# Performance work log

Hardware: AMD Instinct MI355X
Metric: run time of the kernel (lower is better)

## Reference

```python
import jax, jax.numpy as jnp
import numpy as np
from jax import lax

N = 1024          # proposals per image
C = 81            # classes incl. background
F = 1024          # feature dim
K = 100           # detections_per_img
IMG_W, IMG_H = 1216.0, 800.0
SCORE_THRESH = 0.05
NMS_THRESH = 0.5
BBOX_CLIP = float(np.log(1000.0 / 16.0))
WX, WY, WW, WH = 10.0, 10.0, 5.0, 5.0     # BoxCoder default weights


def setup_inputs() -> dict:
    key = jax.random.key(0)
    k1, k2, k3, k4, k5 = jax.random.split(key, 5)
    class_logits = jax.random.normal(k1, (N, C), jnp.float32) * 2.0
    box_regression = jax.random.normal(k2, (N, C * 4), jnp.float32) * 0.2
    xy = jax.random.uniform(k3, (N, 2), jnp.float32) * jnp.array([IMG_W * 0.7, IMG_H * 0.7], jnp.float32)
    wh = 16.0 + jax.random.uniform(k4, (N, 2), jnp.float32) * jnp.array([IMG_W * 0.3, IMG_H * 0.3], jnp.float32)
    proposal_boxes = jnp.concatenate([xy, xy + wh], axis=1)  # valid xyxy
    features = jax.random.normal(k5, (N, F), jnp.float32)
    return {"class_logits": class_logits, "box_regression": box_regression,
            "proposal_boxes": proposal_boxes, "features": features}


def _decode(rel, boxes):
    # BoxCoder.decode with weights (10,10,5,5), TO_REMOVE=1. rel:[N,C*4] boxes:[N,4] -> [N,C,4]
    rel = rel.reshape(N, C, 4)
    widths = boxes[:, 2] - boxes[:, 0] + 1.0
    heights = boxes[:, 3] - boxes[:, 1] + 1.0
    ctr_x = boxes[:, 0] + 0.5 * widths
    ctr_y = boxes[:, 1] + 0.5 * heights
    dx = rel[..., 0] / WX
    dy = rel[..., 1] / WY
    dw = jnp.minimum(rel[..., 2] / WW, BBOX_CLIP)
    dh = jnp.minimum(rel[..., 3] / WH, BBOX_CLIP)
    pcx = dx * widths[:, None] + ctr_x[:, None]
    pcy = dy * heights[:, None] + ctr_y[:, None]
    pw = jnp.exp(dw) * widths[:, None]
    ph = jnp.exp(dh) * heights[:, None]
    return jnp.stack([pcx - 0.5 * pw, pcy - 0.5 * ph,
                      pcx + 0.5 * pw - 1.0, pcy + 0.5 * ph - 1.0], axis=-1)


def _clip(b):
    # clip_to_image with TO_REMOVE=1
    x1 = jnp.clip(b[..., 0], 0.0, IMG_W - 1.0)
    y1 = jnp.clip(b[..., 1], 0.0, IMG_H - 1.0)
    x2 = jnp.clip(b[..., 2], 0.0, IMG_W - 1.0)
    y2 = jnp.clip(b[..., 3], 0.0, IMG_H - 1.0)
    return jnp.stack([x1, y1, x2, y2], axis=-1)


def _nms_class(boxes_c, scores_c, valid_c):
    # Sequential hard NMS for one class with fixed shapes. Invalid (below score
    # thresh) boxes can neither be kept nor suppress others.
    s_sort = jnp.where(valid_c, scores_c, -jnp.inf)
    order = jnp.argsort(-s_sort)              # descending score
    b = boxes_c[order]
    v = valid_c[order]
    s = scores_c[order]
    area = (b[:, 2] - b[:, 0] + 1.0) * (b[:, 3] - b[:, 1] + 1.0)
    lt = jnp.maximum(b[:, None, :2], b[None, :, :2])
    rb = jnp.minimum(b[:, None, 2:], b[None, :, 2:])
    whd = jnp.clip(rb - lt + 1.0, 0.0)
    inter = whd[..., 0] * whd[..., 1]
    iou = inter / (area[:, None] + area[None, :] - inter)  # [N,N]
    idx = jnp.arange(N)
    def body(i, keep):
        sup = (iou[i] > NMS_THRESH) & keep[i] & (idx > i)
        return keep & ~sup
    keep = lax.fori_loop(0, N, body, v)
    return b, order, jnp.where(keep, s, -1.0)


def reference(class_logits, box_regression, proposal_boxes, features):
    probs = jax.nn.softmax(class_logits, axis=-1)          # [N,C]
    dec = _clip(_decode(box_regression, proposal_boxes))    # [N,C,4]
    boxes_cls = jnp.transpose(dec[:, 1:, :], (1, 0, 2))     # [C-1,N,4] (skip background)
    scores_cls = probs[:, 1:].T                             # [C-1,N]
    valid = scores_cls > SCORE_THRESH
    b_s, order, s_kept = jax.vmap(_nms_class)(boxes_cls, scores_cls, valid)
    flat_s = s_kept.reshape(-1)                             # [(C-1)*N]
    top_s, top_i = lax.top_k(flat_s, K)
    cls_i = top_i // N
    pos_i = top_i % N
    boxes_out = b_s[cls_i, pos_i]                           # [K,4]
    orig = order[cls_i, pos_i]                              # original proposal idx
    feat_out = features[orig]                               # [K,F]
    labels = cls_i + 1
    ok = top_s > 0.0
    scores_out = jnp.where(ok, top_s, 0.0)
    boxes_out = jnp.where(ok[:, None], boxes_out, 0.0)
    feat_out = jnp.where(ok[:, None], feat_out, 0.0)
    labels = jnp.where(ok, labels, 0)
    return boxes_out, scores_out, feat_out, labels
```

## Files before the change

kernel.cpp:

```cpp
#include <hip/hip_runtime.h>
#include <math.h>

#define N 1024
#define C 81
#define F 1024
#define K 100
#define NC1 80
#define MAXC (NC1 * N)
#define HBASE 0x3D00
#define HSIZE 1024
#define SELCAP 2048

#define SCORE_THRESH 0.05f
#define NMS_THRESH   0.5f
#define BBOX_CLIP    4.135166556742356f
#define IMG_W1       1215.0f
#define IMG_H1       799.0f

typedef unsigned long long u64;
typedef unsigned int u32;

__device__ float4 decode_box(const float* __restrict__ pboxes,
                             const float* __restrict__ boxreg, int idx, int cl)
{
    float4 pb = ((const float4*)pboxes)[idx];
    float4 r  = *(const float4*)(boxreg + (size_t)idx * (C * 4) + cl * 4);
    float w  = pb.z - pb.x + 1.0f, h = pb.w - pb.y + 1.0f;
    float cx = pb.x + 0.5f * w,  cy = pb.y + 0.5f * h;
    float dx = r.x / 10.0f, dy = r.y / 10.0f;
    float dw = fminf(r.z / 5.0f, BBOX_CLIP);
    float dh = fminf(r.w / 5.0f, BBOX_CLIP);
    float pcx = dx * w + cx, pcy = dy * h + cy;
    float pw = expf(dw) * w, ph = expf(dh) * h;
    float x1 = pcx - 0.5f * pw,        y1 = pcy - 0.5f * ph;
    float x2 = pcx + 0.5f * pw - 1.0f, y2 = pcy + 0.5f * ph - 1.0f;
    x1 = fminf(fmaxf(x1, 0.0f), IMG_W1);
    y1 = fminf(fmaxf(y1, 0.0f), IMG_H1);
    x2 = fminf(fmaxf(x2, 0.0f), IMG_W1);
    y2 = fminf(fmaxf(y2, 0.0f), IMG_H1);
    return make_float4(x1, y1, x2, y2);
}

__global__ __launch_bounds__(256) void k_softmax(
    const float* __restrict__ logits, float2* __restrict__ ms,
    int* __restrict__ hist, int* __restrict__ counter)
{
    int gid = blockIdx.x * 256 + threadIdx.x;
    if (gid < HSIZE) hist[gid] = 0;
    if (gid == 0) *counter = 0;

    int n = blockIdx.x * 4 + (threadIdx.x >> 6);
    int t = threadIdx.x & 63;

    float v1 = logits[n * C + t];
    float v2 = (t < C - 64) ? logits[n * C + 64 + t] : -INFINITY;
    float m = fmaxf(v1, v2);
    for (int off = 32; off; off >>= 1) m = fmaxf(m, __shfl_xor(m, off));
    float e1 = expf(v1 - m);
    float e2 = (t < C - 64) ? expf(v2 - m) : 0.0f;
    float s = e1 + e2;
    for (int off = 32; off; off >>= 1) s += __shfl_xor(s, off);

    if (t == 0) ms[n] = make_float2(m, s);
}

__global__ __launch_bounds__(256) void k_class(
    const float* __restrict__ logits, const float* __restrict__ boxreg,
    const float* __restrict__ pboxes, const float2* __restrict__ ms,
    u64* __restrict__ ckey, float4* __restrict__ cbox, int* __restrict__ corig,
    int* __restrict__ hist, int* __restrict__ counter)
{
    int c = blockIdx.x;
    int cl = c + 1;
    int t = threadIdx.x;
    __shared__ u64    skey64[N];
    __shared__ int    scnt[256];
    __shared__ float4 sbox[N];
    __shared__ float  sarea[N];
    __shared__ int    skeep[N];

    float2 p0 = ms[t],       p1 = ms[t + 256];
    float2 p2 = ms[t + 512], p3 = ms[t + 768];
    float s0 = expf(logits[(t      ) * C + cl] - p0.x) / p0.y;
    float s1 = expf(logits[(t + 256) * C + cl] - p1.x) / p1.y;
    float s2 = expf(logits[(t + 512) * C + cl] - p2.x) / p2.y;
    float s3 = expf(logits[(t + 768) * C + cl] - p3.x) / p3.y;
    int f0 = s0 > SCORE_THRESH, f1 = s1 > SCORE_THRESH;
    int f2 = s2 > SCORE_THRESH, f3 = s3 > SCORE_THRESH;
    int mycount = f0 + f1 + f2 + f3;
    scnt[t] = mycount;
    __syncthreads();
    for (int off = 1; off < 256; off <<= 1) {
        int v = scnt[t];
        int a = (t >= off) ? scnt[t - off] : 0;
        __syncthreads();
        scnt[t] = v + a;
        __syncthreads();
    }
    int base = scnt[t] - mycount;
    int V = scnt[255];
    {
        int pos = base;
        if (f0) skey64[pos++] = ((u64)__float_as_uint(s0) << 32) | (u32)~(u32)(t);
        if (f1) skey64[pos++] = ((u64)__float_as_uint(s1) << 32) | (u32)~(u32)(t + 256);
        if (f2) skey64[pos++] = ((u64)__float_as_uint(s2) << 32) | (u32)~(u32)(t + 512);
        if (f3) skey64[pos++] = ((u64)__float_as_uint(s3) << 32) | (u32)~(u32)(t + 768);
    }
    __syncthreads();
    if (V == 0) return;

    if (V <= 64) {
        if (t < 64) {
            int lane = t;
            u64 key = (lane < V) ? skey64[lane] : 0ull;
            for (int k = 2; k <= 64; k <<= 1) {
                for (int j = k >> 1; j > 0; j >>= 1) {
                    u64 other = __shfl_xor(key, j);
                    bool takeMax = (((lane & j) == 0) == ((lane & k) == 0));
                    bool gt = key > other;
                    key = (takeMax == gt) ? key : other;
                }
            }
            bool act = key != 0ull;
            float4 b = make_float4(0.f, 0.f, 0.f, 0.f);
            float area = 0.0f;
            if (act) {
                int idx = (int)(~(u32)(key & 0xffffffffu));
                b = decode_box(pboxes, boxreg, idx, cl);
                area = (b.z - b.x + 1.0f) * (b.w - b.y + 1.0f);
                cbox[c * N + lane]  = b;
                corig[c * N + lane] = idx;
            }
            int kept = act ? 1 : 0;
            for (int i = 0; i + 1 < V; ++i) {
                int   ki  = __shfl(kept, i);
                float bix = __shfl(b.x, i), biy = __shfl(b.y, i);
                float biz = __shfl(b.z, i), biw = __shfl(b.w, i);
                float ai  = __shfl(area, i);
                if (ki && lane > i && kept) {
                    float lx = fmaxf(bix, b.x), ly = fmaxf(biy, b.y);
                    float rx = fminf(biz, b.z), ry = fminf(biw, b.w);
                    float ww = fmaxf(rx - lx + 1.0f, 0.0f);
                    float hh = fmaxf(ry - ly + 1.0f, 0.0f);
                    float inter = ww * hh;
                    float iou = inter / (ai + area - inter);
                    if (iou > NMS_THRESH) kept = 0;
                }
            }
            if (kept) {
                int pos = atomicAdd(counter, 1);
                u32 sb = (u32)(key >> 32);
                ckey[pos] = ((u64)sb << 32) | (u64)(u32)~(u32)(c * N + lane);
                atomicAdd(&hist[(int)(sb >> 16) - HBASE], 1);
            }
        }
        return;
    }

    int P = 128;
    while (P < V) P <<= 1;
    for (int i = V + t; i < P; i += 256) skey64[i] = 0ull;
    __syncthreads();
    for (int k = 2; k <= P; k <<= 1) {
        for (int j = k >> 1; j > 0; j >>= 1) {
            for (int i = t; i < P; i += 256) {
                int ixj = i ^ j;
                if (ixj > i) {
                    u64 a = skey64[i], bb = skey64[ixj];
                    bool desc = ((i & k) == 0);
                    if (desc ? (a < bb) : (a > bb)) { skey64[i] = bb; skey64[ixj] = a; }
                }
            }
            __syncthreads();
        }
    }
    for (int p = t; p < V; p += 256) {
        int idx = (int)(~(u32)(skey64[p] & 0xffffffffu));
        float4 b = decode_box(pboxes, boxreg, idx, cl);
        sbox[p]  = b;
        sarea[p] = (b.z - b.x + 1.0f) * (b.w - b.y + 1.0f);
        skeep[p] = 1;
        cbox[c * N + p]  = b;
        corig[c * N + p] = idx;
    }
    __syncthreads();
    for (int i = 0; i < V; ++i) {
        if (skeep[i]) {
            float4 bi = sbox[i];
            float  ai = sarea[i];
            for (int j = i + 1 + t; j < V; j += 256) {
                if (skeep[j]) {
                    float4 bj = sbox[j];
                    float lx = fmaxf(bi.x, bj.x), ly = fmaxf(bi.y, bj.y);
                    float rx = fminf(bi.z, bj.z), ry = fminf(bi.w, bj.w);
                    float ww = fmaxf(rx - lx + 1.0f, 0.0f);
                    float hh = fmaxf(ry - ly + 1.0f, 0.0f);
                    float inter = ww * hh;
                    float iou = inter / (ai + sarea[j] - inter);
                    if (iou > NMS_THRESH) skeep[j] = 0;
                }
            }
        }
        __syncthreads();
    }
    for (int p = t; p < V; p += 256) {
        if (skeep[p]) {
            int pos = atomicAdd(counter, 1);
            u32 sb = (u32)(skey64[p] >> 32);
            ckey[pos] = ((u64)sb << 32) | (u64)(u32)~(u32)(c * N + p);
            atomicAdd(&hist[(int)(sb >> 16) - HBASE], 1);
        }
    }
}

__global__ __launch_bounds__(1024) void k_select(
    const int* __restrict__ counter, u64* ckey, const int* __restrict__ hist,
    float* __restrict__ sel_score, int* __restrict__ sel_flat)
{
    int t = threadIdx.x;
    __shared__ u64 keys[SELCAP];
    __shared__ int partial[1024];
    __shared__ int sb_bstar, scount;
    __shared__ u64 wk[16];
    __shared__ int wp[16];

    int M = *counter;
    if (t == 0) { sb_bstar = 0; scount = 0; }

    int lsum = hist[t];
    partial[t] = lsum;
    __syncthreads();
    for (int off = 1; off < 1024; off <<= 1) {
        int v = partial[t];
        int a = (t + off < 1024) ? partial[t + off] : 0;
        __syncthreads();
        partial[t] = v + a;
        __syncthreads();
    }
    int base = partial[t] - lsum;
    if (base < K && base + lsum >= K) sb_bstar = t;
    __syncthreads();
    int bstar = sb_bstar;

    for (int p = t; p < M; p += 1024) {
        u64 kk = ckey[p];
        int b = (int)((kk >> 48) & 0xFFFF) - HBASE;
        if (b >= bstar) {
            int pos = atomicAdd(&scount, 1);
            if (pos < SELCAP) keys[pos] = kk;
        }
    }
    __syncthreads();
    int cnt = scount;

    if (cnt > SELCAP) {
        for (int k = 0; k < K; ++k) {
            u64 key = 0ull; int pos = -1;
            for (int p = t; p < M; p += 1024) {
                u64 kk = ckey[p];
                if (kk > key) { key = kk; pos = p; }
            }
            for (int off = 32; off; off >>= 1) {
                u64 ok2 = __shfl_down(key, off);
                int op = __shfl_down(pos, off);
                if (ok2 > key) { key = ok2; pos = op; }
            }
            if ((t & 63) == 0) { wk[t >> 6] = key; wp[t >> 6] = pos; }
            __syncthreads();
            if (t == 0) {
                for (int w = 1; w < 16; ++w)
                    if (wk[w] > key) { key = wk[w]; pos = wp[w]; }
                if (key != 0ull) {
                    sel_score[k] = __uint_as_float((u32)(key >> 32));
                    sel_flat[k]  = (int)(~(u32)(key & 0xffffffffu));
                    ckey[pos] = 0ull;
                } else { sel_score[k] = 0.0f; sel_flat[k] = 0; }
            }
            __syncthreads();
        }
        return;
    }

    int P = 128;
    while (P < cnt) P <<= 1;
    for (int i = cnt + t; i < P; i += 1024) keys[i] = 0ull;
    __syncthreads();
    for (int k = 2; k <= P; k <<= 1) {
        for (int j = k >> 1; j > 0; j >>= 1) {
            for (int i = t; i < P; i += 1024) {
                int ixj = i ^ j;
                if (ixj > i) {
                    u64 a = keys[i], b = keys[ixj];
                    bool desc = ((i & k) == 0);
                    if (desc ? (a < b) : (a > b)) { keys[i] = b; keys[ixj] = a; }
                }
            }
            __syncthreads();
        }
    }
    if (t < K) {
        u64 key = keys[t];
        sel_score[t] = __uint_as_float((u32)(key >> 32));
        sel_flat[t]  = (int)(~(u32)(key & 0xffffffffu));
    }
}

__global__ __launch_bounds__(256) void k_gather(
    const float* __restrict__ sel_score, const int* __restrict__ sel_flat,
    const int* __restrict__ corig, const float4* __restrict__ cbox,
    const float* __restrict__ feats, float* __restrict__ out)
{
    int k = blockIdx.x, t = threadIdx.x;
    float s = sel_score[k];
    bool ok = s > 0.0f;
    float4 b = make_float4(0.f, 0.f, 0.f, 0.f);
    int label = 0, orig = 0;
    if (ok) {
        int flat = sel_flat[k];
        orig  = corig[flat];
        b     = cbox[flat];
        label = (flat >> 10) + 1;
    }
    if (t == 0) {
        out[k * 4 + 0] = b.x; out[k * 4 + 1] = b.y;
        out[k * 4 + 2] = b.z; out[k * 4 + 3] = b.w;
        out[K * 4 + k] = ok ? s : 0.0f;
        out[K * 4 + K + K * F + k] = (float)label;
    }
    const float4* src = (const float4*)(feats + (size_t)orig * F);
    float4* dst = (float4*)(out + K * 4 + K + (size_t)k * F);
    float4 z = make_float4(0.f, 0.f, 0.f, 0.f);
    if (t < F / 4) dst[t] = ok ? src[t] : z;
}

extern "C" void kernel_launch(void* const* d_in, const int* in_sizes, int n_in,
                              void* d_out, int out_size, void* d_ws, size_t ws_size,
                              hipStream_t stream)
{
    const float* logits = (const float*)d_in[0];
    const float* boxreg = (const float*)d_in[1];
    const float* pboxes = (const float*)d_in[2];
    const float* feats  = (const float*)d_in[3];
    float* out = (float*)d_out;

    char* ws = (char*)d_ws;
    size_t off = 0;
    auto alloc = [&](size_t bytes) {
        size_t cur = off;
        off = (off + bytes + 255) & ~(size_t)255;
        return cur;
    };
    u64*    ckey      = (u64*)   (ws + alloc(sizeof(u64)    * MAXC));
    float4* cbox      = (float4*)(ws + alloc(sizeof(float4) * NC1 * N));
    int*    corig     = (int*)   (ws + alloc(sizeof(int)    * NC1 * N));
    float2* ms        = (float2*)(ws + alloc(sizeof(float2) * N));
    int*    hist      = (int*)   (ws + alloc(sizeof(int)    * HSIZE));
    int*    counter   = (int*)   (ws + alloc(sizeof(int)));
    float*  sel_score = (float*) (ws + alloc(sizeof(float)  * K));
    int*    sel_flat  = (int*)   (ws + alloc(sizeof(int)    * K));

    hipLaunchKernelGGL(k_softmax, dim3(N / 4), dim3(256), 0, stream,
                       logits, ms, hist, counter);
    hipLaunchKernelGGL(k_class, dim3(NC1), dim3(256), 0, stream,
                       logits, boxreg, pboxes, ms, ckey, cbox, corig, hist, counter);
    hipLaunchKernelGGL(k_select, dim3(1), dim3(1024), 0, stream,
                       counter, ckey, hist, sel_score, sel_flat);
    hipLaunchKernelGGL(k_gather, dim3(K), dim3(256), 0, stream,
                       sel_score, sel_flat, corig, cbox, feats, out);
}
```

Measured before the change: 106.1 us.

## Fuse four stage kernels into one cooperative kernel with grid syncs

```diff
diff --git a/kernel.cpp b/kernel.cpp
--- a/kernel.cpp
+++ b/kernel.cpp
@@ -1,5 +1,8 @@
 #include <hip/hip_runtime.h>
+#include <hip/hip_cooperative_groups.h>
 #include <math.h>
+
+namespace cg = cooperative_groups;
 
 #define N 1024
 #define C 81
@@ -10,6 +13,7 @@
 #define HBASE 0x3D00
 #define HSIZE 1024
 #define SELCAP 2048
+#define GRID 256
 
 #define SCORE_THRESH 0.05f
 #define NMS_THRESH   0.5f
@@ -41,296 +45,297 @@
     return make_float4(x1, y1, x2, y2);
 }
 
-__global__ __launch_bounds__(256) void k_softmax(
-    const float* __restrict__ logits, float2* __restrict__ ms,
-    int* __restrict__ hist, int* __restrict__ counter)
-{
-    int gid = blockIdx.x * 256 + threadIdx.x;
-    if (gid < HSIZE) hist[gid] = 0;
-    if (gid == 0) *counter = 0;
-
-    int n = blockIdx.x * 4 + (threadIdx.x >> 6);
-    int t = threadIdx.x & 63;
-
-    float v1 = logits[n * C + t];
-    float v2 = (t < C - 64) ? logits[n * C + 64 + t] : -INFINITY;
-    float m = fmaxf(v1, v2);
-    for (int off = 32; off; off >>= 1) m = fmaxf(m, __shfl_xor(m, off));
-    float e1 = expf(v1 - m);
-    float e2 = (t < C - 64) ? expf(v2 - m) : 0.0f;
-    float s = e1 + e2;
-    for (int off = 32; off; off >>= 1) s += __shfl_xor(s, off);
-
-    if (t == 0) ms[n] = make_float2(m, s);
-}
-
-__global__ __launch_bounds__(256) void k_class(
+__global__ __launch_bounds__(256) void k_fused(
     const float* __restrict__ logits, const float* __restrict__ boxreg,
-    const float* __restrict__ pboxes, const float2* __restrict__ ms,
+    const float* __restrict__ pboxes, const float* __restrict__ feats,
+    float* __restrict__ out,
     u64* __restrict__ ckey, float4* __restrict__ cbox, int* __restrict__ corig,
-    int* __restrict__ hist, int* __restrict__ counter)
-{
-    int c = blockIdx.x;
-    int cl = c + 1;
-    int t = threadIdx.x;
-    __shared__ u64    skey64[N];
-    __shared__ int    scnt[256];
-    __shared__ float4 sbox[N];
-    __shared__ float  sarea[N];
-    __shared__ int    skeep[N];
-
-    float2 p0 = ms[t],       p1 = ms[t + 256];
-    float2 p2 = ms[t + 512], p3 = ms[t + 768];
-    float s0 = expf(logits[(t      ) * C + cl] - p0.x) / p0.y;
-    float s1 = expf(logits[(t + 256) * C + cl] - p1.x) / p1.y;
-    float s2 = expf(logits[(t + 512) * C + cl] - p2.x) / p2.y;
-    float s3 = expf(logits[(t + 768) * C + cl] - p3.x) / p3.y;
-    int f0 = s0 > SCORE_THRESH, f1 = s1 > SCORE_THRESH;
-    int f2 = s2 > SCORE_THRESH, f3 = s3 > SCORE_THRESH;
-    int mycount = f0 + f1 + f2 + f3;
-    scnt[t] = mycount;
-    __syncthreads();
-    for (int off = 1; off < 256; off <<= 1) {
-        int v = scnt[t];
-        int a = (t >= off) ? scnt[t - off] : 0;
-        __syncthreads();
-        scnt[t] = v + a;
-        __syncthreads();
-    }
-    int base = scnt[t] - mycount;
-    int V = scnt[255];
-    {
-        int pos = base;
-        if (f0) skey64[pos++] = ((u64)__float_as_uint(s0) << 32) | (u32)~(u32)(t);
-        if (f1) skey64[pos++] = ((u64)__float_as_uint(s1) << 32) | (u32)~(u32)(t + 256);
-        if (f2) skey64[pos++] = ((u64)__float_as_uint(s2) << 32) | (u32)~(u32)(t + 512);
-        if (f3) skey64[pos++] = ((u64)__float_as_uint(s3) << 32) | (u32)~(u32)(t + 768);
-    }
-    __syncthreads();
-    if (V == 0) return;
-
-    if (V <= 64) {
-        if (t < 64) {
-            int lane = t;
-            u64 key = (lane < V) ? skey64[lane] : 0ull;
-            for (int k = 2; k <= 64; k <<= 1) {
-                for (int j = k >> 1; j > 0; j >>= 1) {
-                    u64 other = __shfl_xor(key, j);
-                    bool takeMax = (((lane & j) == 0) == ((lane & k) == 0));
-                    bool gt = key > other;
-                    key = (takeMax == gt) ? key : other;
-                }
-            }
-            bool act = key != 0ull;
-            float4 b = make_float4(0.f, 0.f, 0.f, 0.f);
-            float area = 0.0f;
-            if (act) {
-                int idx = (int)(~(u32)(key & 0xffffffffu));
-                b = decode_box(pboxes, boxreg, idx, cl);
-                area = (b.z - b.x + 1.0f) * (b.w - b.y + 1.0f);
-                cbox[c * N + lane]  = b;
-                corig[c * N + lane] = idx;
-            }
-            int kept = act ? 1 : 0;
-            for (int i = 0; i + 1 < V; ++i) {
-                int   ki  = __shfl(kept, i);
-                float bix = __shfl(b.x, i), biy = __shfl(b.y, i);
-                float biz = __shfl(b.z, i), biw = __shfl(b.w, i);
-                float ai  = __shfl(area, i);
-                if (ki && lane > i && kept) {
-                    float lx = fmaxf(bix, b.x), ly = fmaxf(biy, b.y);
-                    float rx = fminf(biz, b.z), ry = fminf(biw, b.w);
-                    float ww = fmaxf(rx - lx + 1.0f, 0.0f);
-                    float hh = fmaxf(ry - ly + 1.0f, 0.0f);
-                    float inter = ww * hh;
-                    float iou = inter / (ai + area - inter);
-                    if (iou > NMS_THRESH) kept = 0;
-                }
-            }
-            if (kept) {
-                int pos = atomicAdd(counter, 1);
-                u32 sb = (u32)(key >> 32);
-                ckey[pos] = ((u64)sb << 32) | (u64)(u32)~(u32)(c * N + lane);
-                atomicAdd(&hist[(int)(sb >> 16) - HBASE], 1);
-            }
-        }
-        return;
-    }
-
-    int P = 128;
-    while (P < V) P <<= 1;
-    for (int i = V + t; i < P; i += 256) skey64[i] = 0ull;
-    __syncthreads();
-    for (int k = 2; k <= P; k <<= 1) {
-        for (int j = k >> 1; j > 0; j >>= 1) {
-            for (int i = t; i < P; i += 256) {
-                int ixj = i ^ j;
-                if (ixj > i) {
-                    u64 a = skey64[i], bb = skey64[ixj];
-                    bool desc = ((i & k) == 0);
-                    if (desc ? (a < bb) : (a > bb)) { skey64[i] = bb; skey64[ixj] = a; }
-                }
-            }
-            __syncthreads();
-        }
-    }
-    for (int p = t; p < V; p += 256) {
-        int idx = (int)(~(u32)(skey64[p] & 0xffffffffu));
-        float4 b = decode_box(pboxes, boxreg, idx, cl);
-        sbox[p]  = b;
-        sarea[p] = (b.z - b.x + 1.0f) * (b.w - b.y + 1.0f);
-        skeep[p] = 1;
-        cbox[c * N + p]  = b;
-        corig[c * N + p] = idx;
-    }
-    __syncthreads();
-    for (int i = 0; i < V; ++i) {
-        if (skeep[i]) {
-            float4 bi = sbox[i];
-            float  ai = sarea[i];
-            for (int j = i + 1 + t; j < V; j += 256) {
-                if (skeep[j]) {
-                    float4 bj = sbox[j];
-                    float lx = fmaxf(bi.x, bj.x), ly = fmaxf(bi.y, bj.y);
-                    float rx = fminf(bi.z, bj.z), ry = fminf(bi.w, bj.w);
-                    float ww = fmaxf(rx - lx + 1.0f, 0.0f);
-                    float hh = fmaxf(ry - ly + 1.0f, 0.0f);
-                    float inter = ww * hh;
-                    float iou = inter / (ai + sarea[j] - inter);
-                    if (iou > NMS_THRESH) skeep[j] = 0;
-                }
-            }
-        }
-        __syncthreads();
-    }
-    for (int p = t; p < V; p += 256) {
-        if (skeep[p]) {
-            int pos = atomicAdd(counter, 1);
-            u32 sb = (u32)(skey64[p] >> 32);
-            ckey[pos] = ((u64)sb << 32) | (u64)(u32)~(u32)(c * N + p);
-            atomicAdd(&hist[(int)(sb >> 16) - HBASE], 1);
-        }
-    }
-}
-
-__global__ __launch_bounds__(1024) void k_select(
-    const int* __restrict__ counter, u64* ckey, const int* __restrict__ hist,
+    float2* __restrict__ ms, int* __restrict__ hist, int* __restrict__ counter,
     float* __restrict__ sel_score, int* __restrict__ sel_flat)
 {
-    int t = threadIdx.x;
-    __shared__ u64 keys[SELCAP];
-    __shared__ int partial[1024];
-    __shared__ int sb_bstar, scount;
-    __shared__ u64 wk[16];
-    __shared__ int wp[16];
-
-    int M = *counter;
-    if (t == 0) { sb_bstar = 0; scount = 0; }
-
-    int lsum = hist[t];
-    partial[t] = lsum;
-    __syncthreads();
-    for (int off = 1; off < 1024; off <<= 1) {
-        int v = partial[t];
-        int a = (t + off < 1024) ? partial[t + off] : 0;
-        __syncthreads();
-        partial[t] = v + a;
-        __syncthreads();
+    cg::grid_group grid = cg::this_grid();
+    int t   = threadIdx.x;
+    int blk = blockIdx.x;
+
+    __shared__ __align__(16) char smem[32768];
+    u64*    skey64 = (u64*)smem;
+    float4* sbox   = (float4*)(smem + 8192);
+    float*  sarea  = (float*)(smem + 24576);
+    int*    skeep  = (int*)(smem + 28672);
+    __shared__ int scnt[256];
+    __shared__ int sbstar, scount;
+    __shared__ u64 wk[4];
+    __shared__ int wp[4];
+
+    {
+        int gid = blk * 256 + t;
+        if (gid < HSIZE) hist[gid] = 0;
+        if (gid == 0) *counter = 0;
+
+        int n = blk * 4 + (t >> 6);
+        int l = t & 63;
+        float v1 = logits[n * C + l];
+        float v2 = (l < C - 64) ? logits[n * C + 64 + l] : -INFINITY;
+        float m = fmaxf(v1, v2);
+        for (int off = 32; off; off >>= 1) m = fmaxf(m, __shfl_xor(m, off));
+        float e1 = expf(v1 - m);
+        float e2 = (l < C - 64) ? expf(v2 - m) : 0.0f;
+        float s = e1 + e2;
+        for (int off = 32; off; off >>= 1) s += __shfl_xor(s, off);
+        if (l == 0) ms[n] = make_float2(m, s);
     }
-    int base = partial[t] - lsum;
-    if (base < K && base + lsum >= K) sb_bstar = t;
-    __syncthreads();
-    int bstar = sb_bstar;
-
-    for (int p = t; p < M; p += 1024) {
-        u64 kk = ckey[p];
-        int b = (int)((kk >> 48) & 0xFFFF) - HBASE;
-        if (b >= bstar) {
-            int pos = atomicAdd(&scount, 1);
-            if (pos < SELCAP) keys[pos] = kk;
+    __threadfence();
+    grid.sync();
+
+    if (blk < NC1) {
+        int c = blk, cl = c + 1;
+        float2 p0 = ms[t],       p1 = ms[t + 256];
+        float2 p2 = ms[t + 512], p3 = ms[t + 768];
+        float s0 = expf(logits[(t      ) * C + cl] - p0.x) / p0.y;
+        float s1 = expf(logits[(t + 256) * C + cl] - p1.x) / p1.y;
+        float s2 = expf(logits[(t + 512) * C + cl] - p2.x) / p2.y;
+        float s3 = expf(logits[(t + 768) * C + cl] - p3.x) / p3.y;
+        int f0 = s0 > SCORE_THRESH, f1 = s1 > SCORE_THRESH;
+        int f2 = s2 > SCORE_THRESH, f3 = s3 > SCORE_THRESH;
+        int mycount = f0 + f1 + f2 + f3;
+        scnt[t] = mycount;
+        __syncthreads();
+        for (int off = 1; off < 256; off <<= 1) {
+            int v = scnt[t];
+            int a = (t >= off) ? scnt[t - off] : 0;
+            __syncthreads();
+            scnt[t] = v + a;
+            __syncthreads();
+        }
+        int base = scnt[t] - mycount;
+        int V = scnt[255];
+        {
+            int pos = base;
+            if (f0) skey64[pos++] = ((u64)__float_as_uint(s0) << 32) | (u32)~(u32)(t);
+            if (f1) skey64[pos++] = ((u64)__float_as_uint(s1) << 32) | (u32)~(u32)(t + 256);
+            if (f2) skey64[pos++] = ((u64)__float_as_uint(s2) << 32) | (u32)~(u32)(t + 512);
+            if (f3) skey64[pos++] = ((u64)__float_as_uint(s3) << 32) | (u32)~(u32)(t + 768);
+        }
+        __syncthreads();
+
+        if (V > 0 && V <= 64) {
+            if (t < 64) {
+                int lane = t;
+                u64 key = (lane < V) ? skey64[lane] : 0ull;
+                for (int k = 2; k <= 64; k <<= 1) {
+                    for (int j = k >> 1; j > 0; j >>= 1) {
+                        u64 other = __shfl_xor(key, j);
+                        bool takeMax = (((lane & j) == 0) == ((lane & k) == 0));
+                        bool gt = key > other;
+                        key = (takeMax == gt) ? key : other;
+                    }
+                }
+                bool act = key != 0ull;
+                float4 b = make_float4(0.f, 0.f, 0.f, 0.f);
+                float area = 0.0f;
+                if (act) {
+                    int idx = (int)(~(u32)(key & 0xffffffffu));
+                    b = decode_box(pboxes, boxreg, idx, cl);
+                    area = (b.z - b.x + 1.0f) * (b.w - b.y + 1.0f);
+                    cbox[c * N + lane]  = b;
+                    corig[c * N + lane] = idx;
+                }
+                int kept = act ? 1 : 0;
+                for (int i = 0; i + 1 < V; ++i) {
+                    int   ki  = __shfl(kept, i);
+                    float bix = __shfl(b.x, i), biy = __shfl(b.y, i);
+                    float biz = __shfl(b.z, i), biw = __shfl(b.w, i);
+                    float ai  = __shfl(area, i);
+                    if (ki && lane > i && kept) {
+                        float lx = fmaxf(bix, b.x), ly = fmaxf(biy, b.y);
+                        float rx = fminf(biz, b.z), ry = fminf(biw, b.w);
+                        float ww = fmaxf(rx - lx + 1.0f, 0.0f);
+                        float hh = fmaxf(ry - ly + 1.0f, 0.0f);
+                        float inter = ww * hh;
+                        float iou = inter / (ai + area - inter);
+                        if (iou > NMS_THRESH) kept = 0;
+                    }
+                }
+                if (kept) {
+                    int pos = atomicAdd(counter, 1);
+                    u32 sb = (u32)(key >> 32);
+                    ckey[pos] = ((u64)sb << 32) | (u64)(u32)~(u32)(c * N + lane);
+                    atomicAdd(&hist[(int)(sb >> 16) - HBASE], 1);
+                }
+            }
+        } else if (V > 64) {
+            int P = 128;
+            while (P < V) P <<= 1;
+            for (int i = V + t; i < P; i += 256) skey64[i] = 0ull;
+            __syncthreads();
+            for (int k = 2; k <= P; k <<= 1) {
+                for (int j = k >> 1; j > 0; j >>= 1) {
+                    for (int i = t; i < P; i += 256) {
+                        int ixj = i ^ j;
+                        if (ixj > i) {
+                            u64 a = skey64[i], bb = skey64[ixj];
+                            bool desc = ((i & k) == 0);
+                            if (desc ? (a < bb) : (a > bb)) { skey64[i] = bb; skey64[ixj] = a; }
+                        }
+                    }
+                    __syncthreads();
+                }
+            }
+            for (int p = t; p < V; p += 256) {
+                int idx = (int)(~(u32)(skey64[p] & 0xffffffffu));
+                float4 b = decode_box(pboxes, boxreg, idx, cl);
+                sbox[p]  = b;
+                sarea[p] = (b.z - b.x + 1.0f) * (b.w - b.y + 1.0f);
+                skeep[p] = 1;
+                cbox[c * N + p]  = b;
+                corig[c * N + p] = idx;
+            }
+            __syncthreads();
+            for (int i = 0; i < V; ++i) {
+                if (skeep[i]) {
+                    float4 bi = sbox[i];
+                    float  ai = sarea[i];
+                    for (int j = i + 1 + t; j < V; j += 256) {
+                        if (skeep[j]) {
+                            float4 bj = sbox[j];
+                            float lx = fmaxf(bi.x, bj.x), ly = fmaxf(bi.y, bj.y);
+                            float rx = fminf(bi.z, bj.z), ry = fminf(bi.w, bj.w);
+                            float ww = fmaxf(rx - lx + 1.0f, 0.0f);
+                            float hh = fmaxf(ry - ly + 1.0f, 0.0f);
+                            float inter = ww * hh;
+                            float iou = inter / (ai + sarea[j] - inter);
+                            if (iou > NMS_THRESH) skeep[j] = 0;
+                        }
+                    }
+                }
+                __syncthreads();
+            }
+            for (int p = t; p < V; p += 256) {
+                if (skeep[p]) {
+                    int pos = atomicAdd(counter, 1);
+                    u32 sb = (u32)(skey64[p] >> 32);
+                    ckey[pos] = ((u64)sb << 32) | (u64)(u32)~(u32)(c * N + p);
+                    atomicAdd(&hist[(int)(sb >> 16) - HBASE], 1);
+                }
+            }
         }
     }
-    __syncthreads();
-    int cnt = scount;
-
-    if (cnt > SELCAP) {
-        for (int k = 0; k < K; ++k) {
-            u64 key = 0ull; int pos = -1;
-            for (int p = t; p < M; p += 1024) {
-                u64 kk = ckey[p];
-                if (kk > key) { key = kk; pos = p; }
-            }
-            for (int off = 32; off; off >>= 1) {
-                u64 ok2 = __shfl_down(key, off);
-                int op = __shfl_down(pos, off);
-                if (ok2 > key) { key = ok2; pos = op; }
-            }
-            if ((t & 63) == 0) { wk[t >> 6] = key; wp[t >> 6] = pos; }
-            __syncthreads();
-            if (t == 0) {
-                for (int w = 1; w < 16; ++w)
-                    if (wk[w] > key) { key = wk[w]; pos = wp[w]; }
-                if (key != 0ull) {
-                    sel_score[k] = __uint_as_float((u32)(key >> 32));
-                    sel_flat[k]  = (int)(~(u32)(key & 0xffffffffu));
-                    ckey[pos] = 0ull;
-                } else { sel_score[k] = 0.0f; sel_flat[k] = 0; }
-            }
-            __syncthreads();
-        }
-        return;
+    __threadfence();
+    grid.sync();
+
+    if (blk == 0) {
+        int M = *counter;
+        if (t == 0) { sbstar = 0; scount = 0; }
+
+        int h0 = hist[4 * t], h1 = hist[4 * t + 1];
+        int h2 = hist[4 * t + 2], h3 = hist[4 * t + 3];
+        int gs = h0 + h1 + h2 + h3;
+        scnt[t] = gs;
+        __syncthreads();
+        for (int off = 1; off < 256; off <<= 1) {
+            int v = scnt[t];
+            int a = (t + off < 256) ? scnt[t + off] : 0;
+            __syncthreads();
+            scnt[t] = v + a;
+            __syncthreads();
+        }
+        int above = scnt[t] - gs;
+        int b3 = above, b2 = b3 + h3, b1 = b2 + h2, b0 = b1 + h1;
+        if (b0 < K && b0 + h0 >= K) sbstar = 4 * t;
+        if (b1 < K && b1 + h1 >= K) sbstar = 4 * t + 1;
+        if (b2 < K && b2 + h2 >= K) sbstar = 4 * t + 2;
+        if (b3 < K && b3 + h3 >= K) sbstar = 4 * t + 3;
+        __syncthreads();
+        int bstar = sbstar;
+
+        u64* keys = (u64*)smem;
+        for (int p = t; p < M; p += 256) {
+            u64 kk = ckey[p];
+            int b = (int)((kk >> 48) & 0xFFFF) - HBASE;
+            if (b >= bstar) {
+                int pos = atomicAdd(&scount, 1);
+                if (pos < SELCAP) keys[pos] = kk;
+            }
+        }
+        __syncthreads();
+        int cnt = scount;
+
+        if (cnt > SELCAP) {
+            for (int k = 0; k < K; ++k) {
+                u64 key = 0ull; int pos = -1;
+                for (int p = t; p < M; p += 256) {
+                    u64 kk = ckey[p];
+                    if (kk > key) { key = kk; pos = p; }
+                }
+                for (int off = 32; off; off >>= 1) {
+                    u64 ok2 = __shfl_down(key, off);
+                    int op  = __shfl_down(pos, off);
+                    if (ok2 > key) { key = ok2; pos = op; }
+                }
+                if ((t & 63) == 0) { wk[t >> 6] = key; wp[t >> 6] = pos; }
+                __syncthreads();
+                if (t == 0) {
+                    for (int w = 1; w < 4; ++w)
+                        if (wk[w] > key) { key = wk[w]; pos = wp[w]; }
+                    if (key != 0ull) {
+                        sel_score[k] = __uint_as_float((u32)(key >> 32));
+                        sel_flat[k]  = (int)(~(u32)(key & 0xffffffffu));
+                        ckey[pos] = 0ull;
+                    } else { sel_score[k] = 0.0f; sel_flat[k] = 0; }
+                }
+                __syncthreads();
+            }
+        } else {
+            int P = 128;
+            while (P < cnt) P <<= 1;
+            for (int i = cnt + t; i < P; i += 256) keys[i] = 0ull;
+            __syncthreads();
+            for (int k = 2; k <= P; k <<= 1) {
+                for (int j = k >> 1; j > 0; j >>= 1) {
+                    for (int i = t; i < P; i += 256) {
+                        int ixj = i ^ j;
+                        if (ixj > i) {
+                            u64 a = keys[i], b = keys[ixj];
+                            bool desc = ((i & k) == 0);
+                            if (desc ? (a < b) : (a > b)) { keys[i] = b; keys[ixj] = a; }
+                        }
+                    }
+                    __syncthreads();
+                }
+            }
+            if (t < K) {
+                u64 key = keys[t];
+                sel_score[t] = __uint_as_float((u32)(key >> 32));
+                sel_flat[t]  = (int)(~(u32)(key & 0xffffffffu));
+            }
+        }
     }
-
-    int P = 128;
-    while (P < cnt) P <<= 1;
-    for (int i = cnt + t; i < P; i += 1024) keys[i] = 0ull;
-    __syncthreads();
-    for (int k = 2; k <= P; k <<= 1) {
-        for (int j = k >> 1; j > 0; j >>= 1) {
-            for (int i = t; i < P; i += 1024) {
-                int ixj = i ^ j;
-                if (ixj > i) {
-                    u64 a = keys[i], b = keys[ixj];
-                    bool desc = ((i & k) == 0);
-                    if (desc ? (a < b) : (a > b)) { keys[i] = b; keys[ixj] = a; }
-                }
-            }
-            __syncthreads();
-        }
+    __threadfence();
+    grid.sync();
+
+    if (blk < K) {
+        int k = blk;
+        float s = sel_score[k];
+        bool ok = s > 0.0f;
+        float4 b = make_float4(0.f, 0.f, 0.f, 0.f);
+        int label = 0, orig = 0;
+        if (ok) {
+            int flat = sel_flat[k];
+            orig  = corig[flat];
+            b     = cbox[flat];
+            label = (flat >> 10) + 1;
+        }
+        if (t == 0) {
+            out[k * 4 + 0] = b.x; out[k * 4 + 1] = b.y;
+            out[k * 4 + 2] = b.z; out[k * 4 + 3] = b.w;
+            out[K * 4 + k] = ok ? s : 0.0f;
+            out[K * 4 + K + K * F + k] = (float)label;
+        }
+        const float4* src = (const float4*)(feats + (size_t)orig * F);
+        float4* dst = (float4*)(out + K * 4 + K + (size_t)k * F);
+        float4 z = make_float4(0.f, 0.f, 0.f, 0.f);
+        if (t < F / 4) dst[t] = ok ? src[t] : z;
     }
-    if (t < K) {
-        u64 key = keys[t];
-        sel_score[t] = __uint_as_float((u32)(key >> 32));
-        sel_flat[t]  = (int)(~(u32)(key & 0xffffffffu));
-    }
-}
-
-__global__ __launch_bounds__(256) void k_gather(
-    const float* __restrict__ sel_score, const int* __restrict__ sel_flat,
-    const int* __restrict__ corig, const float4* __restrict__ cbox,
-    const float* __restrict__ feats, float* __restrict__ out)
-{
-    int k = blockIdx.x, t = threadIdx.x;
-    float s = sel_score[k];
-    bool ok = s > 0.0f;
-    float4 b = make_float4(0.f, 0.f, 0.f, 0.f);
-    int label = 0, orig = 0;
-    if (ok) {
-        int flat = sel_flat[k];
-        orig  = corig[flat];
-        b     = cbox[flat];
-        label = (flat >> 10) + 1;
-    }
-    if (t == 0) {
-        out[k * 4 + 0] = b.x; out[k * 4 + 1] = b.y;
-        out[k * 4 + 2] = b.z; out[k * 4 + 3] = b.w;
-        out[K * 4 + k] = ok ? s : 0.0f;
-        out[K * 4 + K + K * F + k] = (float)label;
-    }
-    const float4* src = (const float4*)(feats + (size_t)orig * F);
-    float4* dst = (float4*)(out + K * 4 + K + (size_t)k * F);
-    float4 z = make_float4(0.f, 0.f, 0.f, 0.f);
-    if (t < F / 4) dst[t] = ok ? src[t] : z;
 }
 
 extern "C" void kernel_launch(void* const* d_in, const int* in_sizes, int n_in,
@@ -359,12 +364,12 @@
     float*  sel_score = (float*) (ws + alloc(sizeof(float)  * K));
     int*    sel_flat  = (int*)   (ws + alloc(sizeof(int)    * K));
 
-    hipLaunchKernelGGL(k_softmax, dim3(N / 4), dim3(256), 0, stream,
-                       logits, ms, hist, counter);
-    hipLaunchKernelGGL(k_class, dim3(NC1), dim3(256), 0, stream,
-                       logits, boxreg, pboxes, ms, ckey, cbox, corig, hist, counter);
-    hipLaunchKernelGGL(k_select, dim3(1), dim3(1024), 0, stream,
-                       counter, ckey, hist, sel_score, sel_flat);
-    hipLaunchKernelGGL(k_gather, dim3(K), dim3(256), 0, stream,
-                       sel_score, sel_flat, corig, cbox, feats, out);
+    void* kargs[] = {
+        (void*)&logits, (void*)&boxreg, (void*)&pboxes, (void*)&feats,
+        (void*)&out, (void*)&ckey, (void*)&cbox, (void*)&corig,
+        (void*)&ms, (void*)&hist, (void*)&counter,
+        (void*)&sel_score, (void*)&sel_flat
+    };
+    hipLaunchCooperativeKernel((const void*)k_fused, dim3(GRID), dim3(256),
+                               kargs, 0, stream);
 }
```

Result: slower. 231.3 us (+118.0%).

## Use ballot-based compaction and bitmask suppression-matrix NMS for mid-size classes

Applied to the files above, without the earlier changes.

```diff
diff --git a/kernel.cpp b/kernel.cpp
--- a/kernel.cpp
+++ b/kernel.cpp
@@ -73,11 +73,15 @@
     int c = blockIdx.x;
     int cl = c + 1;
     int t = threadIdx.x;
+    int lane = t & 63, wv = t >> 6;
+
     __shared__ u64    skey64[N];
-    __shared__ int    scnt[256];
     __shared__ float4 sbox[N];
     __shared__ float  sarea[N];
     __shared__ int    skeep[N];
+    __shared__ u64    sup[256][4];
+    __shared__ u64    skw[4];
+    __shared__ int    swc[4];
 
     float2 p0 = ms[t],       p1 = ms[t + 256];
     float2 p2 = ms[t + 512], p3 = ms[t + 768];
@@ -87,31 +91,35 @@
     float s3 = expf(logits[(t + 768) * C + cl] - p3.x) / p3.y;
     int f0 = s0 > SCORE_THRESH, f1 = s1 > SCORE_THRESH;
     int f2 = s2 > SCORE_THRESH, f3 = s3 > SCORE_THRESH;
-    int mycount = f0 + f1 + f2 + f3;
-    scnt[t] = mycount;
-    __syncthreads();
-    for (int off = 1; off < 256; off <<= 1) {
-        int v = scnt[t];
-        int a = (t >= off) ? scnt[t - off] : 0;
-        __syncthreads();
-        scnt[t] = v + a;
-        __syncthreads();
-    }
-    int base = scnt[t] - mycount;
-    int V = scnt[255];
+
+    u64 lmask = (1ull << lane) - 1ull;
+    u64 b0 = __ballot(f0), b1 = __ballot(f1);
+    u64 b2 = __ballot(f2), b3 = __ballot(f3);
+    int wcount = __popcll(b0) + __popcll(b1) + __popcll(b2) + __popcll(b3);
+    if (lane == 0) swc[wv] = wcount;
+    __syncthreads();
+    int w0c = swc[0], w1c = swc[1], w2c = swc[2], w3c = swc[3];
+    int V = w0c + w1c + w2c + w3c;
+    int wbase = (wv > 0 ? w0c : 0) + (wv > 1 ? w1c : 0) + (wv > 2 ? w2c : 0);
     {
-        int pos = base;
-        if (f0) skey64[pos++] = ((u64)__float_as_uint(s0) << 32) | (u32)~(u32)(t);
-        if (f1) skey64[pos++] = ((u64)__float_as_uint(s1) << 32) | (u32)~(u32)(t + 256);
-        if (f2) skey64[pos++] = ((u64)__float_as_uint(s2) << 32) | (u32)~(u32)(t + 512);
-        if (f3) skey64[pos++] = ((u64)__float_as_uint(s3) << 32) | (u32)~(u32)(t + 768);
+        int o0 = wbase;
+        int o1 = o0 + __popcll(b0);
+        int o2 = o1 + __popcll(b1);
+        int o3 = o2 + __popcll(b2);
+        if (f0) skey64[o0 + __popcll(b0 & lmask)] =
+            ((u64)__float_as_uint(s0) << 32) | (u32)~(u32)(t);
+        if (f1) skey64[o1 + __popcll(b1 & lmask)] =
+            ((u64)__float_as_uint(s1) << 32) | (u32)~(u32)(t + 256);
+        if (f2) skey64[o2 + __popcll(b2 & lmask)] =
+            ((u64)__float_as_uint(s2) << 32) | (u32)~(u32)(t + 512);
+        if (f3) skey64[o3 + __popcll(b3 & lmask)] =
+            ((u64)__float_as_uint(s3) << 32) | (u32)~(u32)(t + 768);
     }
     __syncthreads();
     if (V == 0) return;
 
     if (V <= 64) {
         if (t < 64) {
-            int lane = t;
             u64 key = (lane < V) ? skey64[lane] : 0ull;
             for (int k = 2; k <= 64; k <<= 1) {
                 for (int j = k >> 1; j > 0; j >>= 1) {
@@ -157,39 +165,42 @@
         return;
     }
 
-    int P = 128;
-    while (P < V) P <<= 1;
-    for (int i = V + t; i < P; i += 256) skey64[i] = 0ull;
-    __syncthreads();
-    for (int k = 2; k <= P; k <<= 1) {
-        for (int j = k >> 1; j > 0; j >>= 1) {
-            for (int i = t; i < P; i += 256) {
-                int ixj = i ^ j;
-                if (ixj > i) {
-                    u64 a = skey64[i], bb = skey64[ixj];
-                    bool desc = ((i & k) == 0);
-                    if (desc ? (a < bb) : (a > bb)) { skey64[i] = bb; skey64[ixj] = a; }
-                }
-            }
-            __syncthreads();
-        }
-    }
-    for (int p = t; p < V; p += 256) {
-        int idx = (int)(~(u32)(skey64[p] & 0xffffffffu));
-        float4 b = decode_box(pboxes, boxreg, idx, cl);
-        sbox[p]  = b;
-        sarea[p] = (b.z - b.x + 1.0f) * (b.w - b.y + 1.0f);
-        skeep[p] = 1;
-        cbox[c * N + p]  = b;
-        corig[c * N + p] = idx;
-    }
-    __syncthreads();
-    for (int i = 0; i < V; ++i) {
-        if (skeep[i]) {
+    if (V <= 256) {
+        int P = 128;
+        while (P < V) P <<= 1;
+        for (int i = V + t; i < P; i += 256) skey64[i] = 0ull;
+        __syncthreads();
+        for (int k = 2; k <= P; k <<= 1) {
+            for (int j = k >> 1; j > 0; j >>= 1) {
+                if (t < P) {
+                    int i = t, ixj = i ^ j;
+                    if (ixj > i) {
+                        u64 a = skey64[i], bb = skey64[ixj];
+                        bool desc = ((i & k) == 0);
+                        if (desc ? (a < bb) : (a > bb)) { skey64[i] = bb; skey64[ixj] = a; }
+                    }
+                }
+                __syncthreads();
+            }
+        }
+        for (int p = t; p < V; p += 256) {
+            int idx = (int)(~(u32)(skey64[p] & 0xffffffffu));
+            float4 b = decode_box(pboxes, boxreg, idx, cl);
+            sbox[p]  = b;
+            sarea[p] = (b.z - b.x + 1.0f) * (b.w - b.y + 1.0f);
+            cbox[c * N + p]  = b;
+            corig[c * N + p] = idx;
+        }
+        __syncthreads();
+        for (int i = t; i < V; i += 256) {
             float4 bi = sbox[i];
             float  ai = sarea[i];
-            for (int j = i + 1 + t; j < V; j += 256) {
-                if (skeep[j]) {
+            u64 w[4] = {0ull, 0ull, 0ull, 0ull};
+            #pragma unroll
+            for (int g = 0; g < 4; ++g) {
+                int jlo = (i + 1 > g * 64) ? i + 1 : g * 64;
+                int jhi = (V < (g + 1) * 64) ? V : (g + 1) * 64;
+                for (int j = jlo; j < jhi; ++j) {
                     float4 bj = sbox[j];
                     float lx = fmaxf(bi.x, bj.x), ly = fmaxf(bi.y, bj.y);
                     float rx = fminf(bi.z, bj.z), ry = fminf(bi.w, bj.w);
@@ -197,18 +208,118 @@
                     float hh = fmaxf(ry - ly + 1.0f, 0.0f);
                     float inter = ww * hh;
                     float iou = inter / (ai + sarea[j] - inter);
-                    if (iou > NMS_THRESH) skeep[j] = 0;
-                }
-            }
-        }
-        __syncthreads();
-    }
-    for (int p = t; p < V; p += 256) {
-        if (skeep[p]) {
-            int pos = atomicAdd(counter, 1);
-            u32 sb = (u32)(skey64[p] >> 32);
-            ckey[pos] = ((u64)sb << 32) | (u64)(u32)~(u32)(c * N + p);
-            atomicAdd(&hist[(int)(sb >> 16) - HBASE], 1);
+                    if (iou > NMS_THRESH) w[g] |= 1ull << (j & 63);
+                }
+            }
+            sup[i][0] = w[0]; sup[i][1] = w[1];
+            sup[i][2] = w[2]; sup[i][3] = w[3];
+        }
+        __syncthreads();
+        if (t < 64) {
+            u64 r0w0 = sup[t][0], r0w1 = sup[t][1], r0w2 = sup[t][2], r0w3 = sup[t][3];
+            u64 r1w1 = 0, r1w2 = 0, r1w3 = 0;
+            u64 r2w2 = 0, r2w3 = 0;
+            u64 r3w3 = 0;
+            if (64 + t < V)  { r1w1 = sup[64 + t][1];  r1w2 = sup[64 + t][2];  r1w3 = sup[64 + t][3]; }
+            if (128 + t < V) { r2w2 = sup[128 + t][2]; r2w3 = sup[128 + t][3]; }
+            if (192 + t < V) { r3w3 = sup[192 + t][3]; }
+            u64 k0 = ~0ull, k1 = ~0ull, k2 = ~0ull, k3 = ~0ull;
+            {
+                int lim = (V < 64) ? V : 64;
+                for (int i = 0; i < lim; ++i)
+                    if ((k0 >> i) & 1) {
+                        k0 &= ~__shfl(r0w0, i); k1 &= ~__shfl(r0w1, i);
+                        k2 &= ~__shfl(r0w2, i); k3 &= ~__shfl(r0w3, i);
+                    }
+            }
+            if (V > 64) {
+                int lim = (V - 64 < 64) ? V - 64 : 64;
+                for (int i = 0; i < lim; ++i)
+                    if ((k1 >> i) & 1) {
+                        k1 &= ~__shfl(r1w1, i);
+                        k2 &= ~__shfl(r1w2, i); k3 &= ~__shfl(r1w3, i);
+                    }
+            }
+            if (V > 128) {
+                int lim = (V - 128 < 64) ? V - 128 : 64;
+                for (int i = 0; i < lim; ++i)
+                    if ((k2 >> i) & 1) {
+                        k2 &= ~__shfl(r2w2, i); k3 &= ~__shfl(r2w3, i);
+                    }
+            }
+            if (V > 192) {
+                int lim = V - 192;
+                for (int i = 0; i < lim; ++i)
+                    if ((k3 >> i) & 1) k3 &= ~__shfl(r3w3, i);
+            }
+            if (t == 0) { skw[0] = k0; skw[1] = k1; skw[2] = k2; skw[3] = k3; }
+        }
+        __syncthreads();
+        for (int p = t; p < V; p += 256) {
+            if ((skw[p >> 6] >> (p & 63)) & 1ull) {
+                int pos = atomicAdd(counter, 1);
+                u32 sb = (u32)(skey64[p] >> 32);
+                ckey[pos] = ((u64)sb << 32) | (u64)(u32)~(u32)(c * N + p);
+                atomicAdd(&hist[(int)(sb >> 16) - HBASE], 1);
+            }
+        }
+        return;
+    }
+
+    {
+        int P = 512;
+        while (P < V) P <<= 1;
+        for (int i = V + t; i < P; i += 256) skey64[i] = 0ull;
+        __syncthreads();
+        for (int k = 2; k <= P; k <<= 1) {
+            for (int j = k >> 1; j > 0; j >>= 1) {
+                for (int i = t; i < P; i += 256) {
+                    int ixj = i ^ j;
+                    if (ixj > i) {
+                        u64 a = skey64[i], bb = skey64[ixj];
+                        bool desc = ((i & k) == 0);
+                        if (desc ? (a < bb) : (a > bb)) { skey64[i] = bb; skey64[ixj] = a; }
+                    }
+                }
+                __syncthreads();
+            }
+        }
+        for (int p = t; p < V; p += 256) {
+            int idx = (int)(~(u32)(skey64[p] & 0xffffffffu));
+            float4 b = decode_box(pboxes, boxreg, idx, cl);
+            sbox[p]  = b;
+            sarea[p] = (b.z - b.x + 1.0f) * (b.w - b.y + 1.0f);
+            skeep[p] = 1;
+            cbox[c * N + p]  = b;
+            corig[c * N + p] = idx;
+        }
+        __syncthreads();
+        for (int i = 0; i < V; ++i) {
+            if (skeep[i]) {
+                float4 bi = sbox[i];
+                float  ai = sarea[i];
+                for (int j = i + 1 + t; j < V; j += 256) {
+                    if (skeep[j]) {
+                        float4 bj = sbox[j];
+                        float lx = fmaxf(bi.x, bj.x), ly = fmaxf(bi.y, bj.y);
+                        float rx = fminf(bi.z, bj.z), ry = fminf(bi.w, bj.w);
+                        float ww = fmaxf(rx - lx + 1.0f, 0.0f);
+                        float hh = fmaxf(ry - ly + 1.0f, 0.0f);
+                        float inter = ww * hh;
+                        float iou = inter / (ai + sarea[j] - inter);
+                        if (iou > NMS_THRESH) skeep[j] = 0;
+                    }
+                }
+            }
+            __syncthreads();
+        }
+        for (int p = t; p < V; p += 256) {
+            if (skeep[p]) {
+                int pos = atomicAdd(counter, 1);
+                u32 sb = (u32)(skey64[p] >> 32);
+                ckey[pos] = ((u64)sb << 32) | (u64)(u32)~(u32)(c * N + p);
+                atomicAdd(&hist[(int)(sb >> 16) - HBASE], 1);
+            }
         }
     }
 }
```

New measurement: 99.16 us. 6.5% less time.
